# Kernel tuning notes

Hardware: AMD Instinct MI355X
Metric: run time of the kernel (lower is better)

The kernel has to match this reference:

```python
import jax, jax.numpy as jnp
import numpy as np

B, P, C = 256, 64, 31  # batch, patch_size, channel
M = P // 2             # mask_size
WS = M * M             # weight_size = patch_size^2/4


def setup_inputs() -> dict:
    key = jax.random.key(0)
    kx, kw = jax.random.split(key)
    x = jax.random.normal(kx, (B, P, P, C), dtype=jnp.float32)
    w = jax.random.normal(kw, (WS,), dtype=jnp.float32)  # grouped 1x1 conv weight, one scalar per quadrant pixel
    return {"x": x, "w": w}


def reference(x, w):
    b, p, _, c = x.shape
    m = p // 2
    rows = jnp.arange(p)
    ch = jnp.arange(c)
    # per-channel roll: out[b,i,:,ch] = x[b,(i+ch)%p,:,ch]  (shift = -ch along dim 1)
    idx_fwd = (rows[:, None] + ch[None, :]) % p            # [P, C]
    xm = jnp.take_along_axis(x, jnp.broadcast_to(idx_fwd[None, :, None, :], x.shape), axis=1)
    # binarized grouped 1x1 conv == per-pixel sign(w) scaling; same weights on all 4 quadrants
    sb = jnp.sign(w)
    mask = jnp.tile(sb.reshape(m, m), (2, 2))              # [P, P]
    y = xm * mask[None, :, :, None]
    # reverse roll: out[b,i,:,ch] = y[b,(i-ch)%p,:,ch]  (shift = +ch along dim 1)
    idx_bwd = (rows[:, None] - ch[None, :]) % p
    xr = jnp.take_along_axis(y, jnp.broadcast_to(idx_bwd[None, :, None, :], y.shape), axis=1)
    return jnp.sum(xr, axis=3)                             # [B, P, P]
```

## Files before the change

### kernel.cpp

```cpp
#include <hip/hip_runtime.h>


#define CH 31
#define ROW_FLOATS (64 * CH)
#define RPB 4
#define STAGE_F4 ((RPB * ROW_FLOATS) / 4)

typedef const __attribute__((address_space(1))) void* gptr_t;
typedef __attribute__((address_space(3))) void* lptr_t;

__global__ __launch_bounds__(256) void codednet_kernel(
    const float* __restrict__ x,
    const float* __restrict__ w,
    float* __restrict__ out)
{
    __shared__ float4 xs4[STAGE_F4];
    __shared__ float  s_lut[1024];

    const int t   = threadIdx.x;
    const int blk = blockIdx.x;

    const float4* __restrict__ xsrc = (const float4*)x + (size_t)blk * STAGE_F4;
#pragma unroll
    for (int it = 0; it < 7; ++it) {
        const int idx = it * 256 + t;
        __builtin_amdgcn_global_load_lds((gptr_t)(xsrc + idx), (lptr_t)(xs4 + idx), 16, 0, 0);
    }
    if (t < STAGE_F4 - 7 * 256) {
        const int idx = 7 * 256 + t;
        __builtin_amdgcn_global_load_lds((gptr_t)(xsrc + idx), (lptr_t)(xs4 + idx), 16, 0, 0);
    }

    {
        float4 wv = ((const float4*)w)[t];
        float4 sv;
        sv.x = (wv.x > 0.f) ? 1.f : ((wv.x < 0.f) ? -1.f : 0.f);
        sv.y = (wv.y > 0.f) ? 1.f : ((wv.y < 0.f) ? -1.f : 0.f);
        sv.z = (wv.z > 0.f) ? 1.f : ((wv.z < 0.f) ? -1.f : 0.f);
        sv.w = (wv.w > 0.f) ? 1.f : ((wv.w < 0.f) ? -1.f : 0.f);
        ((float4*)s_lut)[t] = sv;
    }
    __syncthreads();

    const int r_local = t >> 6;
    const int j       = t & 63;
    const int i       = (blk * RPB + r_local) & 63;
    const int jm      = j & 31;

    const float* __restrict__ xp = (const float*)xs4 + r_local * ROW_FLOATS + j * CH;

    float a0 = 0.f, a1 = 0.f, a2 = 0.f, a3 = 0.f;
#pragma unroll
    for (int ch = 0; ch < 28; ch += 4) {
        a0 += xp[ch + 0] * s_lut[(((i - ch - 0) & 31) << 5) | jm];
        a1 += xp[ch + 1] * s_lut[(((i - ch - 1) & 31) << 5) | jm];
        a2 += xp[ch + 2] * s_lut[(((i - ch - 2) & 31) << 5) | jm];
        a3 += xp[ch + 3] * s_lut[(((i - ch - 3) & 31) << 5) | jm];
    }
    a0 += xp[28] * s_lut[(((i - 28) & 31) << 5) | jm];
    a1 += xp[29] * s_lut[(((i - 29) & 31) << 5) | jm];
    a2 += xp[30] * s_lut[(((i - 30) & 31) << 5) | jm];

    const float sum = (a0 + a1) + (a2 + a3);
    __builtin_nontemporal_store(sum, &out[(size_t)blk * 256 + t]);
}

extern "C" void kernel_launch(void* const* d_in, const int* in_sizes, int n_in,
                              void* d_out, int out_size, void* d_ws, size_t ws_size,
                              hipStream_t stream) {
    const float* x = (const float*)d_in[0];
    const float* w = (const float*)d_in[1];
    float* out = (float*)d_out;

    const int grid = (256 * 64) / RPB;
    codednet_kernel<<<grid, 256, 0, stream>>>(x, w, out);
}
```

Measured before the change: 181.6 us.

## Process four rows per wave with per-wave LDS staging and prefetch of next row

Each wave now owns one LDS row buffer and loops over four consecutive rows. It copies the current row from LDS into registers, then issues async global-to-LDS loads for the next row before computing, so the load overlaps with compute. The grid shrinks from 4096 to 1024 blocks, which cuts per-block setup such as the sign LUT build. Each wave handles its rows serially, which limits parallelism and may expose load latency because there is only one row buffer per wave.

```diff
diff --git a/kernel.cpp b/kernel.cpp
--- a/kernel.cpp
+++ b/kernel.cpp
@@ -2,34 +2,43 @@
 
 
 #define CH 31
-#define ROW_FLOATS (64 * CH)
-#define RPB 4
-#define STAGE_F4 ((RPB * ROW_FLOATS) / 4)
+#define ROW_F4 496
+#define WAVES_PER_BLOCK 4
+#define ROWS_PER_WAVE 4
+#define NBLOCKS 1024
 
 typedef const __attribute__((address_space(1))) void* gptr_t;
 typedef __attribute__((address_space(3))) void* lptr_t;
+
+__device__ __forceinline__ void stage_row(const float4* __restrict__ src,
+                                          float4* dst, int lane)
+{
+#pragma unroll
+    for (int it = 0; it < 7; ++it) {
+        __builtin_amdgcn_global_load_lds((gptr_t)(src + it * 64 + lane),
+                                         (lptr_t)(dst + it * 64 + lane), 16, 0, 0);
+    }
+    if (lane < ROW_F4 - 7 * 64) {
+        __builtin_amdgcn_global_load_lds((gptr_t)(src + 448 + lane),
+                                         (lptr_t)(dst + 448 + lane), 16, 0, 0);
+    }
+}
 
 __global__ __launch_bounds__(256) void codednet_kernel(
     const float* __restrict__ x,
     const float* __restrict__ w,
     float* __restrict__ out)
 {
-    __shared__ float4 xs4[STAGE_F4];
+    __shared__ float4 xs4[WAVES_PER_BLOCK][ROW_F4];
     __shared__ float  s_lut[1024];
 
-    const int t   = threadIdx.x;
-    const int blk = blockIdx.x;
+    const int t    = threadIdx.x;
+    const int lane = t & 63;
+    const int wl   = t >> 6;
+    const int wid  = blockIdx.x * WAVES_PER_BLOCK + wl;
+    const int row0 = wid * ROWS_PER_WAVE;
 
-    const float4* __restrict__ xsrc = (const float4*)x + (size_t)blk * STAGE_F4;
-#pragma unroll
-    for (int it = 0; it < 7; ++it) {
-        const int idx = it * 256 + t;
-        __builtin_amdgcn_global_load_lds((gptr_t)(xsrc + idx), (lptr_t)(xs4 + idx), 16, 0, 0);
-    }
-    if (t < STAGE_F4 - 7 * 256) {
-        const int idx = 7 * 256 + t;
-        __builtin_amdgcn_global_load_lds((gptr_t)(xsrc + idx), (lptr_t)(xs4 + idx), 16, 0, 0);
-    }
+    stage_row((const float4*)x + (size_t)row0 * ROW_F4, &xs4[wl][0], lane);
 
     {
         float4 wv = ((const float4*)w)[t];
@@ -42,27 +51,41 @@
     }
     __syncthreads();
 
-    const int r_local = t >> 6;
-    const int j       = t & 63;
-    const int i       = (blk * RPB + r_local) & 63;
-    const int jm      = j & 31;
+    const int j  = lane;
+    const int jm = j & 31;
+    const float* __restrict__ xbase = (const float*)&xs4[wl][0] + j * CH;
 
-    const float* __restrict__ xp = (const float*)xs4 + r_local * ROW_FLOATS + j * CH;
+#pragma unroll 1
+    for (int k = 0; k < ROWS_PER_WAVE; ++k) {
+        const int row = row0 + k;
 
-    float a0 = 0.f, a1 = 0.f, a2 = 0.f, a3 = 0.f;
+        asm volatile("s_waitcnt vmcnt(0)" ::: "memory");
+
+        float xv[CH];
 #pragma unroll
-    for (int ch = 0; ch < 28; ch += 4) {
-        a0 += xp[ch + 0] * s_lut[(((i - ch - 0) & 31) << 5) | jm];
-        a1 += xp[ch + 1] * s_lut[(((i - ch - 1) & 31) << 5) | jm];
-        a2 += xp[ch + 2] * s_lut[(((i - ch - 2) & 31) << 5) | jm];
-        a3 += xp[ch + 3] * s_lut[(((i - ch - 3) & 31) << 5) | jm];
+        for (int c = 0; c < CH; ++c) xv[c] = xbase[c];
+        asm volatile("s_waitcnt lgkmcnt(0)" ::: "memory");
+
+        if (k + 1 < ROWS_PER_WAVE) {
+            stage_row((const float4*)x + (size_t)(row + 1) * ROW_F4, &xs4[wl][0], lane);
+        }
+
+        const int i = row & 63;
+        float a0 = 0.f, a1 = 0.f, a2 = 0.f, a3 = 0.f;
+#pragma unroll
+        for (int c = 0; c < 28; c += 4) {
+            a0 += xv[c + 0] * s_lut[(((i - c - 0) & 31) << 5) | jm];
+            a1 += xv[c + 1] * s_lut[(((i - c - 1) & 31) << 5) | jm];
+            a2 += xv[c + 2] * s_lut[(((i - c - 2) & 31) << 5) | jm];
+            a3 += xv[c + 3] * s_lut[(((i - c - 3) & 31) << 5) | jm];
+        }
+        a0 += xv[28] * s_lut[(((i - 28) & 31) << 5) | jm];
+        a1 += xv[29] * s_lut[(((i - 29) & 31) << 5) | jm];
+        a2 += xv[30] * s_lut[(((i - 30) & 31) << 5) | jm];
+
+        const float sum = (a0 + a1) + (a2 + a3);
+        __builtin_nontemporal_store(sum, &out[(size_t)row * 64 + j]);
     }
-    a0 += xp[28] * s_lut[(((i - 28) & 31) << 5) | jm];
-    a1 += xp[29] * s_lut[(((i - 29) & 31) << 5) | jm];
-    a2 += xp[30] * s_lut[(((i - 30) & 31) << 5) | jm];
-
-    const float sum = (a0 + a1) + (a2 + a3);
-    __builtin_nontemporal_store(sum, &out[(size_t)blk * 256 + t]);
 }
 
 extern "C" void kernel_launch(void* const* d_in, const int* in_sizes, int n_in,
@@ -72,6 +95,5 @@
     const float* w = (const float*)d_in[1];
     float* out = (float*)d_out;
 
-    const int grid = (256 * 64) / RPB;
-    codednet_kernel<<<grid, 256, 0, stream>>>(x, w, out);
+    codednet_kernel<<<NBLOCKS, 256, 0, stream>>>(x, w, out);
 }
```

After: 184.5 us. No clear change (+1.6%).
